# Optimization experiments

Measured on AMD Instinct MI355X. Metric: run time of the kernel, lower is better.

## Reference

```python
import jax, jax.numpy as jnp
import numpy as np

ALPHA = 3.0      # tanhalpha
K = 10           # subgraph_size (overridden to 10 in __init__)
PROP_ALPHA = 0.05
DEPTH = 2        # gcn_depth
NUM_FEAT = 2


def _build_graph(emb1, emb2, w1, b1, w2, b2):
    # MTGNN graph_constructor: directed adjacency + row-wise top-k sparsification
    n1 = jnp.tanh(ALPHA * (emb1 @ w1 + b1))
    n2 = jnp.tanh(ALPHA * (emb2 @ w2 + b2))
    a = n1 @ n2.T - n2 @ n1.T
    adj = jax.nn.relu(jnp.tanh(ALPHA * a))          # [N, N]
    _, idx = jax.lax.top_k(adj, K)                  # keep top-K per row
    N = adj.shape[0]
    mask = jnp.zeros_like(adj).at[jnp.arange(N)[:, None], idx].set(1.0)
    return adj * mask


def _norm_adj(adj):
    a = adj + jnp.eye(adj.shape[0], dtype=adj.dtype)
    return a / a.sum(axis=1, keepdims=True)


def _mixprop(x, a_norm, w, b):
    # x: [B, C, N, L]; multi-hop diffusion then 1x1 conv over stacked hops
    h = x
    outs = [x]
    for _ in range(DEPTH):
        h = PROP_ALPHA * x + (1.0 - PROP_ALPHA) * jnp.einsum('bcwl,vw->bcvl', h, a_norm)
        outs.append(h)
    ho = jnp.concatenate(outs, axis=1)              # [B, (D+1)C, N, L]
    return jnp.einsum('bcnl,oc->bonl', ho, w) + b[None, :, None, None]


def _conv1x1(x, w, b):
    # 1x1 Conv2d over channel dim of [B, C, N, L]
    return jnp.einsum('bcnl,oc->bonl', x, w) + b[None, :, None, None]


def _forward(history_data, node_emb_u, T_i_D_emb, D_i_W_emb,
             gc_emb1, gc_emb2, gc_w1, gc_b1, gc_w2, gc_b2,
             W_emb, b_emb, Wg1, bg1, Wg2, bg2, Wsc, bsc,
             mix1_w, mix1_b, mix2_w, mix2_b,
             Wtf1, btf1, Wtf2, btf2, Wec1, bec1, Wec2, bec2,
             Wfc1, bfc1, Wfc2, bfc2, Wec3, bec3):
    # --- prepare inputs ---
    tid_idx = (history_data[..., NUM_FEAT] * 288.0).astype(jnp.int32)   # [B,T,N]
    diw_idx = history_data[..., NUM_FEAT + 1].astype(jnp.int32)
    tid = T_i_D_emb[tid_idx]                                            # [B,T,N,TE]
    diw = D_i_W_emb[diw_idx]                                            # [B,T,N,TE]
    hd = history_data[..., :NUM_FEAT]                                   # [B,T,N,F]

    adj = _build_graph(gc_emb1, gc_emb2, gc_w1, gc_b1, gc_w2, gc_b2)    # [N,N]

    hd = hd @ W_emb + b_emb                                             # [B,T,N,H]
    B, T, N, H = hd.shape

    # --- decouple gate 1 ---
    nu = jnp.broadcast_to(node_emb_u[None, None], (B, T, N, node_emb_u.shape[-1]))
    g_in = jnp.concatenate([nu, tid, diw], axis=-1)                     # [B,T,N,64]
    gate = jax.nn.sigmoid(jax.nn.relu(g_in @ Wg1 + bg1) @ Wg2 + bg2)    # [B,T,N,H]
    x1 = gate * hd
    x2 = hd - x1
    gated = jnp.concatenate([x1, x2], axis=-1)                          # [B,T,N,2H]

    # start conv acts on the T(=12) dim as channels
    x1 = jax.nn.relu(jnp.einsum('btnh,ot->bonh', x1, Wsc) + bsc[None, :, None, None])
    x2 = jax.nn.relu(jnp.einsum('btnh,ot->bonh', x2, Wsc) + bsc[None, :, None, None])

    aN = _norm_adj(adj)
    aTN = _norm_adj(adj.T)
    outs = []
    for i in range(2):
        H1 = _mixprop(x1, aN, mix1_w[i], mix1_b[i]) + _mixprop(x1, aTN, mix2_w[i], mix2_b[i])
        H2 = _mixprop(x2, aN, mix1_w[i], mix1_b[i]) + _mixprop(x2, aTN, mix2_w[i], mix2_b[i])
        outs.append(H1)
        outs.append(H2)
    out = jnp.concatenate(outs, axis=-1)                                # [B,32,N,4H]

    # TFModule: 2-layer MLP on last dim (dropout = identity in eval)
    x = jax.nn.relu(out @ Wtf1 + btf1) @ Wtf2 + btf2                    # [B,32,N,4H]

    x = jax.nn.relu(_conv1x1(x, Wec1, bec1))                            # [B,128,N,4H]
    x = _conv1x1(x, Wec2, bec2)                                         # [B,12,N,4H]

    fh = jnp.concatenate([gated, x, tid, diw, hd], axis=-1)             # [B,12,N,472]
    f = jax.nn.relu(jax.nn.relu(fh) @ Wfc1 + bfc1) @ Wfc2 + bfc2        # [B,12,N,gap]
    f = _conv1x1(f, Wec3, bec3)                                         # [B,4,N,gap]
    f = jnp.transpose(f, (0, 2, 1, 3)).reshape(B, N, -1)                # [B,N,12]
    return f


def setup_inputs() -> dict:
    key = jax.random.key(0)
    ks = iter(jax.random.split(key, 48))
    def p(*shape, s=0.1):
        return (jax.random.normal(next(ks), shape, jnp.float32) * s)
    B, T, N, F_, H, ND, TE = 8, 12, 1024, 2, 64, 40, 12
    feat = jax.random.normal(next(ks), (B, T, N, F_), jnp.float32)
    tid = jax.random.uniform(next(ks), (B, T, N, 1), jnp.float32)
    diw = jax.random.randint(next(ks), (B, T, N, 1), 0, 7).astype(jnp.float32)
    history_data = jnp.concatenate([feat, tid, diw], axis=-1)
    return {
        'history_data': history_data,
        'node_emb_u': p(N, ND), 'T_i_D_emb': p(288, TE), 'D_i_W_emb': p(7, TE),
        'gc_emb1': p(N, ND), 'gc_emb2': p(N, ND),
        'gc_w1': p(ND, ND), 'gc_b1': jnp.zeros((ND,), jnp.float32),
        'gc_w2': p(ND, ND), 'gc_b2': jnp.zeros((ND,), jnp.float32),
        'W_emb': p(F_, H), 'b_emb': jnp.zeros((H,), jnp.float32),
        'Wg1': p(ND + 2 * TE, 64), 'bg1': jnp.zeros((64,), jnp.float32),
        'Wg2': p(64, H), 'bg2': jnp.zeros((H,), jnp.float32),
        'Wsc': p(32, T), 'bsc': jnp.zeros((32,), jnp.float32),
        'mix1_w': p(2, 32, 96), 'mix1_b': jnp.zeros((2, 32), jnp.float32),
        'mix2_w': p(2, 32, 96), 'mix2_b': jnp.zeros((2, 32), jnp.float32),
        'Wtf1': p(4 * H, 256, s=0.05), 'btf1': jnp.zeros((256,), jnp.float32),
        'Wtf2': p(256, 4 * H, s=0.05), 'btf2': jnp.zeros((4 * H,), jnp.float32),
        'Wec1': p(128, 32), 'bec1': jnp.zeros((128,), jnp.float32),
        'Wec2': p(12, 128), 'bec2': jnp.zeros((12,), jnp.float32),
        'Wfc1': p(472, 512, s=0.05), 'bfc1': jnp.zeros((512,), jnp.float32),
        'Wfc2': p(512, 3, s=0.05), 'bfc2': jnp.zeros((3,), jnp.float32),
        'Wec3': p(4, 12), 'bec3': jnp.zeros((4,), jnp.float32),
    }


def reference(history_data, node_emb_u, T_i_D_emb, D_i_W_emb,
              gc_emb1, gc_emb2, gc_w1, gc_b1, gc_w2, gc_b2,
              W_emb, b_emb, Wg1, bg1, Wg2, bg2, Wsc, bsc,
              mix1_w, mix1_b, mix2_w, mix2_b,
              Wtf1, btf1, Wtf2, btf2, Wec1, bec1, Wec2, bec2,
              Wfc1, bfc1, Wfc2, bfc2, Wec3, bec3):
    return _forward(history_data, node_emb_u, T_i_D_emb, D_i_W_emb,
                    gc_emb1, gc_emb2, gc_w1, gc_b1, gc_w2, gc_b2,
                    W_emb, b_emb, Wg1, bg1, Wg2, bg2, Wsc, bsc,
                    mix1_w, mix1_b, mix2_w, mix2_b,
                    Wtf1, btf1, Wtf2, btf2, Wec1, bec1, Wec2, bec2,
                    Wfc1, bfc1, Wfc2, bfc2, Wec3, bec3)
```

## Files before the change

kernel.cpp:

```cpp
#include <hip/hip_runtime.h>
#include <math.h>

constexpr int ROWS_PER_B = 12 * 1024;

constexpr size_t F_N1 = 0;
constexpr size_t F_N2 = 40960;
constexpr size_t F_ANVAL = 81920;
constexpr size_t F_ROWVAL = 93184;
constexpr size_t F_COLSUM = 103424;
constexpr size_t F_INVCS = 104448;
constexpr size_t F_ATVAL = 105472;
constexpr size_t I_ANIDX = 115712;
constexpr size_t I_ROWIDX = 126976;
constexpr size_t I_COLCNT = 137216;
constexpr size_t I_COLOFF = 138240;
constexpr size_t I_COLFILL = 139265;
constexpr size_t I_ATIDX = 140289;
constexpr size_t F_W1P = 151552;
constexpr size_t F_W2P = 184320;
constexpr size_t F_WFCP = 217088;
constexpr size_t F_WEC1P = 339968;
constexpr size_t F_WEC2P = 342016;
constexpr size_t F_WMWP = 343040;
constexpr size_t GRAPH_FLOATS = 524288;

constexpr size_t PB_GATED = (size_t)ROWS_PER_B * 128 / 2;
constexpr size_t PB_HD = (size_t)ROWS_PER_B * 64 / 2;
constexpr size_t PB_X = (size_t)32 * 1024 * 64 / 2;
constexpr size_t PB_MIX = (size_t)32 * 1024 * 256 / 2;
constexpr size_t PB_TOTAL = PB_GATED + PB_HD + 5 * PB_X + PB_MIX;

typedef __attribute__((ext_vector_type(8))) short bf16x8;
typedef __attribute__((ext_vector_type(4))) float f32x4;

__device__ __forceinline__ unsigned short f2bf(float f) {
    unsigned u = __float_as_uint(f);
    unsigned r = (u + 0x7fffu + ((u >> 16) & 1u)) >> 16;
    return (unsigned short)r;
}
__device__ __forceinline__ float bf2f(unsigned short h) {
    return __uint_as_float((unsigned)h << 16);
}
__device__ __forceinline__ void unpack8(uint4 raw, float* f) {
    f[0] = bf2f((unsigned short)(raw.x & 0xffff)); f[1] = bf2f((unsigned short)(raw.x >> 16));
    f[2] = bf2f((unsigned short)(raw.y & 0xffff)); f[3] = bf2f((unsigned short)(raw.y >> 16));
    f[4] = bf2f((unsigned short)(raw.z & 0xffff)); f[5] = bf2f((unsigned short)(raw.z >> 16));
    f[6] = bf2f((unsigned short)(raw.w & 0xffff)); f[7] = bf2f((unsigned short)(raw.w >> 16));
}
__device__ __forceinline__ uint4 pack8(const float* f) {
    uint4 r;
    r.x = f2bf(f[0]) | ((unsigned)f2bf(f[1]) << 16);
    r.y = f2bf(f[2]) | ((unsigned)f2bf(f[3]) << 16);
    r.z = f2bf(f[4]) | ((unsigned)f2bf(f[5]) << 16);
    r.w = f2bf(f[6]) | ((unsigned)f2bf(f[7]) << 16);
    return r;
}
__device__ __forceinline__ bf16x8 relu8(bf16x8 v) {
#pragma unroll
    for (int j = 0; j < 8; j++) {
        unsigned short u = (unsigned short)v[j];
        v[j] = (short)((u >> 15) ? 0 : u);
    }
    return v;
}


__global__ void k_init(int* cnt, int* fill, float* csum) {
    int t = blockIdx.x * 256 + threadIdx.x;
    if (t < 1024) { cnt[t] = 0; fill[t] = 0; csum[t] = 0.f; }
}

__global__ void k_embed(const float* e1, const float* e2, const float* w1, const float* b1,
                        const float* w2, const float* b2, float* n1, float* n2) {
    int idx = blockIdx.x * 256 + threadIdx.x;
    if (idx >= 81920) return;
    int m = idx / 40960, rem = idx - m * 40960;
    int i = rem / 40, j = rem - i * 40;
    const float* e = m ? e2 : e1;
    const float* w = m ? w2 : w1;
    const float* bv = m ? b2 : b1;
    float a = bv[j];
    for (int k = 0; k < 40; k++) a += e[i * 40 + k] * w[k * 40 + j];
    (m ? n2 : n1)[i * 40 + j] = tanhf(3.0f * a);
}

__global__ __launch_bounds__(256) void k_adj(const float* n1, const float* n2,
        float* aN_val, int* aN_idx, float* row_val, int* row_idx,
        int* col_cnt, float* col_sum) {
    __shared__ float arow[1024];
    __shared__ float n1v[40], n2v[40];
    __shared__ float rv[256];
    __shared__ int ri[256];
    __shared__ float topv[10];
    __shared__ int topi[10];
    int v = blockIdx.x, t = threadIdx.x;
    if (t < 40) { n1v[t] = n1[v * 40 + t]; n2v[t] = n2[v * 40 + t]; }
    __syncthreads();
    for (int j = t; j < 1024; j += 256) {
        float d1 = 0.f, d2 = 0.f;
        for (int k = 0; k < 40; k++) {
            d1 += n1v[k] * n2[j * 40 + k];
            d2 += n2v[k] * n1[j * 40 + k];
        }
        float a = tanhf(3.0f * (d1 - d2));
        arow[j] = a > 0.f ? a : 0.f;
    }
    __syncthreads();
    for (int r = 0; r < 10; r++) {
        float bv = -1.f; int bi = 1 << 30;
        for (int j = t; j < 1024; j += 256) {
            float x = arow[j];
            if (x > bv || (x == bv && j < bi)) { bv = x; bi = j; }
        }
        rv[t] = bv; ri[t] = bi;
        __syncthreads();
        for (int s = 128; s > 0; s >>= 1) {
            if (t < s) {
                float ov = rv[t + s]; int oi = ri[t + s];
                if (ov > rv[t] || (ov == rv[t] && oi < ri[t])) { rv[t] = ov; ri[t] = oi; }
            }
            __syncthreads();
        }
        if (t == 0) { topv[r] = rv[0]; topi[r] = ri[0]; arow[ri[0]] = -1.f; }
        __syncthreads();
    }
    if (t == 0) {
        float s = 1.f;
        for (int r = 0; r < 10; r++) s += topv[r];
        float inv = 1.f / s;
        for (int r = 0; r < 10; r++) {
            aN_idx[v * 11 + r] = topi[r];
            aN_val[v * 11 + r] = topv[r] * inv;
            row_idx[v * 10 + r] = topi[r];
            row_val[v * 10 + r] = topv[r];
            atomicAdd(&col_cnt[topi[r]], 1);
            atomicAdd(&col_sum[topi[r]], topv[r]);
        }
        aN_idx[v * 11 + 10] = v;
        aN_val[v * 11 + 10] = inv;
    }
}

__global__ __launch_bounds__(1024) void k_scan(const int* cnt, int* off,
                                               const float* csum, float* inv) {
    __shared__ int tmp[1024];
    int t = threadIdx.x;
    tmp[t] = cnt[t];
    __syncthreads();
    for (int s = 1; s < 1024; s <<= 1) {
        int v = 0;
        if (t >= s) v = tmp[t - s];
        __syncthreads();
        tmp[t] += v;
        __syncthreads();
    }
    off[t + 1] = tmp[t];
    if (t == 0) off[0] = 0;
    inv[t] = 1.0f / (csum[t] + 1.0f);
}

__global__ void k_scatter(const int* row_idx, const float* row_val, const int* off,
                          int* fill, int* aT_idx, float* aT_val) {
    int e = blockIdx.x * 256 + threadIdx.x;
    if (e >= 10240) return;
    int v = e / 10;
    int j = row_idx[e];
    int pos = off[j] + atomicAdd(&fill[j], 1);
    aT_idx[pos] = v;
    aT_val[pos] = row_val[e];
}

__global__ void k_packw(const float* W, unsigned short* out) {
    int id = blockIdx.x * 256 + threadIdx.x;
    if (id >= 8192) return;
    int lane = id & 63, rest = id >> 6;
    int nb = rest & 15, kb = rest >> 4;
    int krow = kb * 32 + (lane >> 4) * 8;
    int col = nb * 16 + (lane & 15);
    unsigned short v[8];
#pragma unroll
    for (int j = 0; j < 8; j++) v[j] = f2bf(W[(size_t)(krow + j) * 256 + col]);
#pragma unroll
    for (int j = 0; j < 8; j++) out[(size_t)id * 8 + j] = v[j];
}

__global__ void k_packfc(const float* W, unsigned short* out) {
    int id = blockIdx.x * 256 + threadIdx.x;
    if (id >= 30720) return;
    int lane = id & 63, rest = id >> 6;
    int nb = rest & 31, kb = rest >> 5;
    int k0 = kb * 32 + (lane >> 4) * 8;
    int col = nb * 16 + (lane & 15);
    unsigned short v[8];
#pragma unroll
    for (int j = 0; j < 8; j++) {
        int k = k0 + j;
        v[j] = (k < 472) ? f2bf(W[(size_t)k * 512 + col]) : (unsigned short)0;
    }
#pragma unroll
    for (int j = 0; j < 8; j++) out[(size_t)id * 8 + j] = v[j];
}

__global__ void k_packec(const float* W1, const float* W2,
                         unsigned short* o1, unsigned short* o2) {
    int id = blockIdx.x * 256 + threadIdx.x;
    if (id < 512) {
        int mt = id >> 6, lane = id & 63;
        int o = mt * 16 + (lane & 15);
        int c0 = (lane >> 4) * 8;
#pragma unroll
        for (int j = 0; j < 8; j++)
            o1[(size_t)id * 8 + j] = f2bf(W1[o * 32 + c0 + j]);
    } else if (id < 768) {
        int id2 = id - 512;
        int kb = id2 >> 6, lane = id2 & 63;
        int p = lane & 15;
        int k0 = kb * 32 + (lane >> 4) * 8;
#pragma unroll
        for (int j = 0; j < 8; j++)
            o2[(size_t)id2 * 8 + j] = (p < 12) ? f2bf(W2[p * 128 + k0 + j])
                                               : (unsigned short)0;
    }
}

__global__ void k_packmw(const float* mw1, const float* mw2, unsigned short* out) {
    int id = blockIdx.x * 256 + threadIdx.x;
    if (id >= 1536) return;
    int f = id >> 6, lane = id & 63;
    int kb = f >> 2, rt = f & 3;
    int row = rt * 16 + (lane & 15);
    int ph = (kb >= 3) ? 1 : 0;
    int kloc = (kb - ph * 3) * 32 + (lane >> 4) * 8;
    const float* mw = ph ? mw2 : mw1;
#pragma unroll
    for (int j = 0; j < 8; j++)
        out[(size_t)id * 8 + j] = f2bf(mw[row * 96 + kloc + j]);
}


__global__ __launch_bounds__(256) void k_gate(const float* hist, const float* nodeu,
        const float* tide, const float* diwe,
        const float* Wg1, const float* bg1, const float* Wg2, const float* bg2,
        const float* Wemb, const float* bemb, unsigned short* gated, unsigned short* hd_emb) {
    __shared__ float w1[4096], w2[4096];
    __shared__ float gin[4][64], hid[4][64];
    __shared__ float sb1[64], sb2[64], we[128], be[64];
    int t = threadIdx.x;
    for (int i = t; i < 4096; i += 256) { w1[i] = Wg1[i]; w2[i] = Wg2[i]; }
    if (t < 64) { sb1[t] = bg1[t]; sb2[t] = bg2[t]; be[t] = bemb[t]; }
    if (t < 128) we[t] = Wemb[t];
    int r = t >> 6, lane = t & 63;
    int row = blockIdx.x * 4 + r;
    int n = row & 1023;
    const float* hrow = hist + (size_t)row * 4;
    float f0 = hrow[0], f1 = hrow[1];
    int tid_i = (int)(hrow[2] * 288.0f);
    int diw_i = (int)hrow[3];
    float g;
    if (lane < 40) g = nodeu[n * 40 + lane];
    else if (lane < 52) g = tide[tid_i * 12 + lane - 40];
    else g = diwe[diw_i * 12 + lane - 52];
    gin[r][lane] = g;
    __syncthreads();
    float acc = sb1[lane];
    for (int k = 0; k < 64; k++) acc += gin[r][k] * w1[k * 64 + lane];
    hid[r][lane] = acc > 0.f ? acc : 0.f;
    __syncthreads();
    acc = sb2[lane];
    for (int k = 0; k < 64; k++) acc += hid[r][k] * w2[k * 64 + lane];
    float gate = 1.f / (1.f + expf(-acc));
    float hd = f0 * we[lane] + f1 * we[64 + lane] + be[lane];
    float x1 = gate * hd;
    gated[(size_t)row * 128 + lane] = f2bf(x1);
    gated[(size_t)row * 128 + 64 + lane] = f2bf(hd - x1);
    hd_emb[(size_t)row * 64 + lane] = f2bf(hd);
}

__global__ __launch_bounds__(256) void k_wsc(const unsigned short* gated, const float* Wsc,
                                             const float* bsc, unsigned short* xs, int xoff) {
    __shared__ float w[384];
    __shared__ float sb[32];
    int t = threadIdx.x;
    if (t < 384) w[t] = Wsc[t];
    if (t < 32) sb[t] = bsc[t];
    __syncthreads();
    int idx = blockIdx.x * 256 + t;
    int h = idx & 63, n = (idx >> 6) & 1023, b = idx >> 16;
    float xv[12];
#pragma unroll
    for (int tt = 0; tt < 12; tt++)
        xv[tt] = bf2f(gated[(size_t)((b * 12 + tt) * 1024 + n) * 128 + xoff + h]);
#pragma unroll
    for (int o = 0; o < 32; o++) {
        float a = sb[o];
#pragma unroll
        for (int tt = 0; tt < 12; tt++) a += xv[tt] * w[o * 12 + tt];
        xs[(size_t)((b * 32 + o) * 1024 + n) * 64 + h] = f2bf(a > 0.f ? a : 0.f);
    }
}

__global__ __launch_bounds__(256) void k_spmm2(unsigned short* out1, unsigned short* out2,
        const unsigned short* x, const unsigned short* hin1, const unsigned short* hin2,
        const int* aN_idx, const float* aN_val,
        const int* aT_idx, const float* aT_val,
        const int* off, const float* inv_cs) {
    int nper = gridDim.x >> 3;
    int bid = (blockIdx.x & 7) * nper + (blockIdx.x >> 3);
    int t = threadIdx.x;
    int l8 = t & 7, r = t >> 3;
    int g = bid * 32 + r;
    int v = g & 1023, bc = g >> 10;
    size_t rowoff = (size_t)bc * 65536;
    float hv[8];
    const unsigned short* base1 = hin1 + rowoff;
    float s1[8];
#pragma unroll
    for (int j = 0; j < 8; j++) s1[j] = 0.f;
#pragma unroll
    for (int e = 0; e < 11; e++) {
        int w = aN_idx[v * 11 + e];
        float a = aN_val[v * 11 + e];
        uint4 raw = *(const uint4*)(base1 + (size_t)w * 64 + l8 * 8);
        unpack8(raw, hv);
#pragma unroll
        for (int j = 0; j < 8; j++) s1[j] += a * hv[j];
    }
    const unsigned short* base2 = hin2 + rowoff;
    float s2[8];
    {
        uint4 raw = *(const uint4*)(base2 + (size_t)v * 64 + l8 * 8);
        unpack8(raw, s2);
        int e0 = off[v], e1 = off[v + 1];
        for (int e = e0; e < e1; e++) {
            int w = aT_idx[e];
            float a = aT_val[e];
            uint4 rw = *(const uint4*)(base2 + (size_t)w * 64 + l8 * 8);
            unpack8(rw, hv);
#pragma unroll
            for (int j = 0; j < 8; j++) s2[j] += a * hv[j];
        }
        float ic = inv_cs[v];
#pragma unroll
        for (int j = 0; j < 8; j++) s2[j] *= ic;
    }
    uint4 xr = *(const uint4*)(x + (size_t)g * 64 + l8 * 8);
    float xv[8];
    unpack8(xr, xv);
    float o1[8], o2[8];
#pragma unroll
    for (int j = 0; j < 8; j++) {
        float xb = 0.05f * xv[j];
        o1[j] = xb + 0.95f * s1[j];
        o2[j] = xb + 0.95f * s2[j];
    }
    *(uint4*)(out1 + (size_t)g * 64 + l8 * 8) = pack8(o1);
    *(uint4*)(out2 + (size_t)g * 64 + l8 * 8) = pack8(o2);
}

__global__ __launch_bounds__(256) void k_proj(const unsigned short* xs,
        const unsigned short* h1, const unsigned short* h2,
        const unsigned short* h1b, const unsigned short* h2b,
        const unsigned short* mwp, const float* m1b, const float* m2b,
        unsigned short* mix, int xp) {
    __shared__ unsigned short Bf[24 * 64 * 8];
    int t = threadIdx.x;
    int wave = t >> 6, l = t & 63;
    int lr = l & 15, lg = l >> 4;
    int b = blockIdx.x >> 10, n = blockIdx.x & 1023;
#pragma unroll
    for (int i = 0; i < 6; i++) {
        int f = wave * 6 + i;
        int kb = f >> 2, nt = f & 3;
        int ph = (kb >= 3) ? 1 : 0;
        int q = kb - ph * 3;
        const unsigned short* Hq = (q == 0) ? xs : (q == 1 ? (ph ? h1b : h1)
                                                           : (ph ? h2b : h2));
        const unsigned short* src = Hq + ((size_t)(b * 32 + lg * 8) * 1024 + n) * 64
                                       + nt * 16 + lr;
        bf16x8 v;
#pragma unroll
        for (int j = 0; j < 8; j++)
            v[j] = (short)src[(size_t)j * 65536];
        *(bf16x8*)(Bf + ((size_t)f * 64 + l) * 8) = v;
    }
    __syncthreads();
    f32x4 acc[4];
#pragma unroll
    for (int nt = 0; nt < 4; nt++) {
        f32x4 c;
#pragma unroll
        for (int r = 0; r < 4; r++) {
            int row = wave * 16 + lg * 4 + r;
            c[r] = m1b[row] + m2b[row];
        }
        acc[nt] = c;
    }
#pragma unroll
    for (int kb = 0; kb < 6; kb++) {
        bf16x8 af = *(const bf16x8*)(mwp + (size_t)((kb * 4 + wave) * 64 + l) * 8);
#pragma unroll
        for (int nt = 0; nt < 4; nt++) {
            bf16x8 bfv = *(const bf16x8*)(Bf + ((size_t)(kb * 4 + nt) * 64 + l) * 8);
            acc[nt] = __builtin_amdgcn_mfma_f32_16x16x32_bf16(af, bfv, acc[nt], 0, 0, 0);
        }
    }
#pragma unroll
    for (int nt = 0; nt < 4; nt++)
#pragma unroll
        for (int r = 0; r < 4; r++) {
            int row = wave * 16 + lg * 4 + r;
            int i2 = row >> 5, o = row & 31;
            mix[(size_t)((b * 32 + o) * 1024 + n) * 256 + (i2 * 2 + xp) * 64 + nt * 16 + lr]
                = f2bf(acc[nt][r]);
        }
}

__global__ __launch_bounds__(256) void k_tf(unsigned short* mix, const unsigned short* W1p,
                                            const float* B1, const unsigned short* W2p,
                                            const float* B2) {
    __shared__ unsigned short Abuf[32 * 256];
    __shared__ unsigned short Hbuf[32 * 256];
    int t = threadIdx.x;
    int wave = t >> 6, l = t & 63;
    size_t row0 = (size_t)blockIdx.x * 32;
    const uint4* src = (const uint4*)(mix + row0 * 256);
#pragma unroll
    for (int it = 0; it < 4; it++) {
        int f = t + it * 256;
        uint4 raw = src[f];
        int e = f * 8, row = e >> 8, col = e & 255;
        int byte = (row * 512 + col * 2) ^ ((row & 7) << 4);
        *(uint4*)((char*)Abuf + byte) = raw;
    }
    __syncthreads();
    int colg0 = wave * 64;
    int lr = l & 15, lg = l >> 4;
    f32x4 acc[2][4];
#pragma unroll
    for (int nb = 0; nb < 4; nb++) {
        float bv = B1[colg0 + nb * 16 + lr];
        f32x4 c; c[0] = bv; c[1] = bv; c[2] = bv; c[3] = bv;
        acc[0][nb] = c; acc[1][nb] = c;
    }
#pragma unroll
    for (int kb = 0; kb < 8; kb++) {
        int k2 = (kb * 32 + lg * 8) * 2;
        int by0 = (lr * 512 + k2) ^ ((lr & 7) << 4);
        int by1 = ((16 + lr) * 512 + k2) ^ ((lr & 7) << 4);
        bf16x8 a0 = *(const bf16x8*)((char*)Abuf + by0);
        bf16x8 a1 = *(const bf16x8*)((char*)Abuf + by1);
#pragma unroll
        for (int nb = 0; nb < 4; nb++) {
            int nbg = wave * 4 + nb;
            bf16x8 bw = *(const bf16x8*)(W1p + (size_t)((kb * 16 + nbg) * 64 + l) * 8);
            acc[0][nb] = __builtin_amdgcn_mfma_f32_16x16x32_bf16(a0, bw, acc[0][nb], 0, 0, 0);
            acc[1][nb] = __builtin_amdgcn_mfma_f32_16x16x32_bf16(a1, bw, acc[1][nb], 0, 0, 0);
        }
    }
#pragma unroll
    for (int rb = 0; rb < 2; rb++)
#pragma unroll
        for (int nb = 0; nb < 4; nb++)
#pragma unroll
            for (int r = 0; r < 4; r++) {
                int row = rb * 16 + lg * 4 + r;
                int col = colg0 + nb * 16 + lr;
                unsigned short h = f2bf(fmaxf(acc[rb][nb][r], 0.f));
                int byte = (row * 512 + col * 2) ^ ((row & 7) << 4);
                *(unsigned short*)((char*)Hbuf + byte) = h;
            }
    __syncthreads();
#pragma unroll
    for (int nb = 0; nb < 4; nb++) {
        float bv = B2[colg0 + nb * 16 + lr];
        f32x4 c; c[0] = bv; c[1] = bv; c[2] = bv; c[3] = bv;
        acc[0][nb] = c; acc[1][nb] = c;
    }
#pragma unroll
    for (int kb = 0; kb < 8; kb++) {
        int k2 = (kb * 32 + lg * 8) * 2;
        int by0 = (lr * 512 + k2) ^ ((lr & 7) << 4);
        int by1 = ((16 + lr) * 512 + k2) ^ ((lr & 7) << 4);
        bf16x8 a0 = *(const bf16x8*)((char*)Hbuf + by0);
        bf16x8 a1 = *(const bf16x8*)((char*)Hbuf + by1);
#pragma unroll
        for (int nb = 0; nb < 4; nb++) {
            int nbg = wave * 4 + nb;
            bf16x8 bw = *(const bf16x8*)(W2p + (size_t)((kb * 16 + nbg) * 64 + l) * 8);
            acc[0][nb] = __builtin_amdgcn_mfma_f32_16x16x32_bf16(a0, bw, acc[0][nb], 0, 0, 0);
            acc[1][nb] = __builtin_amdgcn_mfma_f32_16x16x32_bf16(a1, bw, acc[1][nb], 0, 0, 0);
        }
    }
#pragma unroll
    for (int rb = 0; rb < 2; rb++)
#pragma unroll
        for (int nb = 0; nb < 4; nb++)
#pragma unroll
            for (int r = 0; r < 4; r++) {
                int row = rb * 16 + lg * 4 + r;
                int col = colg0 + nb * 16 + lr;
                mix[(row0 + row) * 256 + col] = f2bf(acc[rb][nb][r]);
            }
}

__global__ __launch_bounds__(256) void k_ec(const unsigned short* tfo,
        const unsigned short* W1p, const float* B1,
        const unsigned short* W2p, const float* B2, unsigned short* eco) {
    __shared__ unsigned short Hl[4 * 64 * 48];
    int t = threadIdx.x;
    int wave = t >> 6, l = t & 63;
    int lr = l & 15, lg = l >> 4;
    int b = blockIdx.x >> 10, n = blockIdx.x & 1023;
    int lbase = wave * 64;
    unsigned short* myH = Hl + wave * 3072;
    const unsigned short* xb = tfo + ((size_t)(b * 32) * 1024 + n) * 256;
    bf16x8 xf[4];
#pragma unroll
    for (int nt = 0; nt < 4; nt++) {
        int ll = lbase + nt * 16 + lr;
        bf16x8 v;
#pragma unroll
        for (int j = 0; j < 8; j++)
            v[j] = (short)xb[(size_t)(lg * 8 + j) * 262144 + ll];
        xf[nt] = v;
    }
    f32x4 d2[4];
    {
        f32x4 c;
#pragma unroll
        for (int r = 0; r < 4; r++) {
            int p = lg * 4 + r;
            c[r] = (p < 12) ? B2[p] : 0.f;
        }
#pragma unroll
        for (int nt = 0; nt < 4; nt++) d2[nt] = c;
    }
#pragma unroll
    for (int ch = 0; ch < 4; ch++) {
        f32x4 h[2][4];
#pragma unroll
        for (int mt = 0; mt < 2; mt++) {
            f32x4 c;
#pragma unroll
            for (int r = 0; r < 4; r++) c[r] = B1[ch * 32 + mt * 16 + lg * 4 + r];
#pragma unroll
            for (int nt = 0; nt < 4; nt++) h[mt][nt] = c;
        }
#pragma unroll
        for (int mt = 0; mt < 2; mt++) {
            bf16x8 aw = *(const bf16x8*)(W1p + (size_t)((ch * 2 + mt) * 64 + l) * 8);
#pragma unroll
            for (int nt = 0; nt < 4; nt++)
                h[mt][nt] = __builtin_amdgcn_mfma_f32_16x16x32_bf16(aw, xf[nt], h[mt][nt], 0, 0, 0);
        }
#pragma unroll
        for (int mt = 0; mt < 2; mt++)
#pragma unroll
            for (int nt = 0; nt < 4; nt++) {
                unsigned lo = f2bf(fmaxf(h[mt][nt][0], 0.f)) |
                              ((unsigned)f2bf(fmaxf(h[mt][nt][1], 0.f)) << 16);
                unsigned hi = f2bf(fmaxf(h[mt][nt][2], 0.f)) |
                              ((unsigned)f2bf(fmaxf(h[mt][nt][3], 0.f)) << 16);
                uint2 pk; pk.x = lo; pk.y = hi;
                *(uint2*)(myH + (nt * 16 + lr) * 48 + mt * 16 + lg * 4) = pk;
            }
        bf16x8 aw2 = *(const bf16x8*)(W2p + (size_t)(ch * 64 + l) * 8);
#pragma unroll
        for (int nt = 0; nt < 4; nt++) {
            bf16x8 hf = *(const bf16x8*)(myH + (nt * 16 + lr) * 48 + lg * 8);
            d2[nt] = __builtin_amdgcn_mfma_f32_16x16x32_bf16(aw2, hf, d2[nt], 0, 0, 0);
        }
    }
#pragma unroll
    for (int nt = 0; nt < 4; nt++)
#pragma unroll
        for (int r = 0; r < 4; r++) {
            int p = lg * 4 + r;
            if (p < 12) {
                int ll = lbase + nt * 16 + lr;
                eco[((size_t)(b * 12 + p) * 1024 + n) * 256 + ll] = f2bf(d2[nt][r]);
            }
        }
}

__global__ __launch_bounds__(256, 3) void k_fc(const unsigned short* gated,
        const unsigned short* eco, const unsigned short* hd_emb,
        const float* hist, const float* tide, const float* diwe,
        const unsigned short* W1p, const float* B1, const float* W2,
        float* pbuf) {
    int t = threadIdx.x;
    int wave = t >> 6, l = t & 63;
    int lr = l & 15, lg = l >> 4;
    int row0 = blockIdx.x * 16;
    int grow = row0 + lr;
    int n = grow & 1023, bt = grow >> 10;
    int b = bt / 12, tt = bt - b * 12;
    const unsigned short* gptr = gated + (size_t)grow * 128;
    const unsigned short* eptr = eco + (size_t)((b * 12 + tt) * 1024 + n) * 256;
    const unsigned short* hptr = hd_emb + (size_t)grow * 64;
    int tid_i = (int)(hist[(size_t)grow * 4 + 2] * 288.0f);
    int diw_i = (int)hist[(size_t)grow * 4 + 3];
    bf16x8 af[15];
#pragma unroll
    for (int kb = 0; kb < 15; kb++) {
        int off = kb * 32 + lg * 8;
        if (kb <= 3) {
            af[kb] = relu8(*(const bf16x8*)(gptr + off));
        } else if (kb <= 11) {
            af[kb] = relu8(*(const bf16x8*)(eptr + off - 128));
        } else if (kb == 12) {
            bf16x8 v;
#pragma unroll
            for (int j = 0; j < 8; j++) {
                int k = off + j;
                float x;
                if (k < 396) x = tide[tid_i * 12 + k - 384];
                else if (k < 408) x = diwe[diw_i * 12 + k - 396];
                else x = bf2f(hptr[k - 408]);
                v[j] = (short)f2bf(fmaxf(x, 0.f));
            }
            af[kb] = v;
        } else if (kb == 13) {
            af[kb] = relu8(*(const bf16x8*)(hptr + off - 408));
        } else {
            if (lg < 3) af[kb] = relu8(*(const bf16x8*)(hptr + off - 408));
            else {
                bf16x8 z;
#pragma unroll
                for (int j = 0; j < 8; j++) z[j] = 0;
                af[kb] = z;
            }
        }
    }
    __builtin_amdgcn_sched_barrier(0);
    int colg0 = wave * 128;
    f32x4 acc[8];
#pragma unroll
    for (int nb = 0; nb < 8; nb++) {
        float bv = B1[colg0 + nb * 16 + lr];
        f32x4 c; c[0] = bv; c[1] = bv; c[2] = bv; c[3] = bv;
        acc[nb] = c;
    }
#pragma unroll
    for (int kb = 0; kb < 15; kb++) {
#pragma unroll
        for (int nb = 0; nb < 8; nb++) {
            bf16x8 bw = *(const bf16x8*)(W1p + (size_t)((kb * 32 + wave * 8 + nb) * 64 + l) * 8);
            acc[nb] = __builtin_amdgcn_mfma_f32_16x16x32_bf16(af[kb], bw, acc[nb], 0, 0, 0);
        }
    }
    float p[4][3];
#pragma unroll
    for (int r = 0; r < 4; r++) { p[r][0] = 0.f; p[r][1] = 0.f; p[r][2] = 0.f; }
#pragma unroll
    for (int nb = 0; nb < 8; nb++) {
        int col = colg0 + nb * 16 + lr;
        float w0 = W2[col * 3], w1 = W2[col * 3 + 1], w2 = W2[col * 3 + 2];
#pragma unroll
        for (int r = 0; r < 4; r++) {
            float h = fmaxf(acc[nb][r], 0.f);
            p[r][0] += h * w0; p[r][1] += h * w1; p[r][2] += h * w2;
        }
    }
#pragma unroll
    for (int off = 8; off >= 1; off >>= 1)
#pragma unroll
        for (int r = 0; r < 4; r++) {
            p[r][0] += __shfl_xor(p[r][0], off);
            p[r][1] += __shfl_xor(p[r][1], off);
            p[r][2] += __shfl_xor(p[r][2], off);
        }
    if (lr == 0) {
#pragma unroll
        for (int r = 0; r < 4; r++) {
            size_t gr = (size_t)(row0 + lg * 4 + r);
#pragma unroll
            for (int pp = 0; pp < 3; pp++)
                pbuf[gr * 12 + wave * 3 + pp] = p[r][pp];
        }
    }
}

__global__ void k_ec3(const float* pbuf, const float* B2, const float* W, const float* bv,
                      float* out) {
    int idx = blockIdx.x * 256 + threadIdx.x;
    int l = idx % 3;
    int rest = idx / 3;
    int o = rest & 3;
    int n = (rest >> 2) & 1023;
    int b = rest >> 12;
    float s = bv[o];
#pragma unroll
    for (int c = 0; c < 12; c++) {
        const float* pb = pbuf + ((size_t)(b * 12 + c) * 1024 + n) * 12;
        float fv = B2[l] + pb[l] + pb[3 + l] + pb[6 + l] + pb[9 + l];
        s += fv * W[o * 12 + c];
    }
    out[idx] = s;
}

extern "C" void kernel_launch(void* const* d_in, const int* in_sizes, int n_in,
                              void* d_out, int out_size, void* d_ws, size_t ws_size,
                              hipStream_t stream) {
    const float* hist = (const float*)d_in[0];
    const float* node_emb_u = (const float*)d_in[1];
    const float* T_i_D_emb = (const float*)d_in[2];
    const float* D_i_W_emb = (const float*)d_in[3];
    const float* gc_emb1 = (const float*)d_in[4];
    const float* gc_emb2 = (const float*)d_in[5];
    const float* gc_w1 = (const float*)d_in[6];
    const float* gc_b1 = (const float*)d_in[7];
    const float* gc_w2 = (const float*)d_in[8];
    const float* gc_b2 = (const float*)d_in[9];
    const float* W_emb = (const float*)d_in[10];
    const float* b_emb = (const float*)d_in[11];
    const float* Wg1 = (const float*)d_in[12];
    const float* bg1 = (const float*)d_in[13];
    const float* Wg2 = (const float*)d_in[14];
    const float* bg2 = (const float*)d_in[15];
    const float* Wsc = (const float*)d_in[16];
    const float* bsc = (const float*)d_in[17];
    const float* mix1_w = (const float*)d_in[18];
    const float* mix1_b = (const float*)d_in[19];
    const float* mix2_w = (const float*)d_in[20];
    const float* mix2_b = (const float*)d_in[21];
    const float* Wtf1 = (const float*)d_in[22];
    const float* btf1 = (const float*)d_in[23];
    const float* Wtf2 = (const float*)d_in[24];
    const float* btf2 = (const float*)d_in[25];
    const float* Wec1 = (const float*)d_in[26];
    const float* bec1 = (const float*)d_in[27];
    const float* Wec2 = (const float*)d_in[28];
    const float* bec2 = (const float*)d_in[29];
    const float* Wfc1 = (const float*)d_in[30];
    const float* bfc1 = (const float*)d_in[31];
    const float* Wfc2 = (const float*)d_in[32];
    const float* bfc2 = (const float*)d_in[33];
    const float* Wec3 = (const float*)d_in[34];
    const float* bec3 = (const float*)d_in[35];

    float* ws = (float*)d_ws;
    float* n1 = ws + F_N1;
    float* n2 = ws + F_N2;
    float* aN_val = ws + F_ANVAL;
    float* row_val = ws + F_ROWVAL;
    float* col_sum = ws + F_COLSUM;
    float* inv_cs = ws + F_INVCS;
    float* aT_val = ws + F_ATVAL;
    int* aN_idx = (int*)(ws + I_ANIDX);
    int* row_idx = (int*)(ws + I_ROWIDX);
    int* col_cnt = (int*)(ws + I_COLCNT);
    int* col_off = (int*)(ws + I_COLOFF);
    int* col_fill = (int*)(ws + I_COLFILL);
    int* aT_idx = (int*)(ws + I_ATIDX);
    unsigned short* w1p = (unsigned short*)(ws + F_W1P);
    unsigned short* w2p = (unsigned short*)(ws + F_W2P);
    unsigned short* wfcp = (unsigned short*)(ws + F_WFCP);
    unsigned short* wec1p = (unsigned short*)(ws + F_WEC1P);
    unsigned short* wec2p = (unsigned short*)(ws + F_WEC2P);
    unsigned short* wmwp = (unsigned short*)(ws + F_WMWP);

    size_t avail = ws_size / 4;
    int CB = 8;
    while (CB > 1 && GRAPH_FLOATS + (size_t)CB * PB_TOTAL > avail) CB >>= 1;
    int nchunk = 8 / CB;

    unsigned short* gated = (unsigned short*)(ws + GRAPH_FLOATS);
    unsigned short* hd_emb = (unsigned short*)(ws + GRAPH_FLOATS + (size_t)CB * PB_GATED);
    unsigned short* xs = (unsigned short*)(ws + GRAPH_FLOATS + (size_t)CB * (PB_GATED + PB_HD));
    unsigned short* h1 = xs + (size_t)CB * PB_X * 2;
    unsigned short* h2 = h1 + (size_t)CB * PB_X * 2;
    unsigned short* h1b = h2 + (size_t)CB * PB_X * 2;
    unsigned short* h2b = h1b + (size_t)CB * PB_X * 2;
    unsigned short* mix = h2b + (size_t)CB * PB_X * 2;
    unsigned short* eco = xs;
    float* fbuf = (float*)h2b;

    k_init<<<4, 256, 0, stream>>>(col_cnt, col_fill, col_sum);
    k_embed<<<320, 256, 0, stream>>>(gc_emb1, gc_emb2, gc_w1, gc_b1, gc_w2, gc_b2, n1, n2);
    k_adj<<<1024, 256, 0, stream>>>(n1, n2, aN_val, aN_idx, row_val, row_idx, col_cnt, col_sum);
    k_scan<<<1, 1024, 0, stream>>>(col_cnt, col_off, col_sum, inv_cs);
    k_scatter<<<40, 256, 0, stream>>>(row_idx, row_val, col_off, col_fill, aT_idx, aT_val);
    k_packw<<<32, 256, 0, stream>>>(Wtf1, w1p);
    k_packw<<<32, 256, 0, stream>>>(Wtf2, w2p);
    k_packfc<<<120, 256, 0, stream>>>(Wfc1, wfcp);
    k_packec<<<3, 256, 0, stream>>>(Wec1, Wec2, wec1p, wec2p);
    k_packmw<<<6, 256, 0, stream>>>(mix1_w, mix2_w, wmwp);

    for (int ch = 0; ch < nchunk; ch++) {
        const float* hist_c = hist + (size_t)ch * CB * ROWS_PER_B * 4;
        float* out_c = (float*)d_out + (size_t)ch * CB * ROWS_PER_B;

        k_gate<<<CB * 3072, 256, 0, stream>>>(hist_c, node_emb_u, T_i_D_emb, D_i_W_emb,
                                              Wg1, bg1, Wg2, bg2, W_emb, b_emb, gated, hd_emb);
        for (int xp = 0; xp < 2; xp++) {
            k_wsc<<<CB * 256, 256, 0, stream>>>(gated, Wsc, bsc, xs, xp * 64);
            k_spmm2<<<CB * 1024, 256, 0, stream>>>(h1, h1b, xs, xs, xs,
                                                   aN_idx, aN_val, aT_idx, aT_val,
                                                   col_off, inv_cs);
            k_spmm2<<<CB * 1024, 256, 0, stream>>>(h2, h2b, xs, h1, h1b,
                                                   aN_idx, aN_val, aT_idx, aT_val,
                                                   col_off, inv_cs);
            k_proj<<<CB * 1024, 256, 0, stream>>>(xs, h1, h2, h1b, h2b,
                                                  wmwp, mix1_b, mix2_b, mix, xp);
        }
        k_tf<<<CB * 1024, 256, 0, stream>>>(mix, w1p, btf1, w2p, btf2);
        k_ec<<<CB * 1024, 256, 0, stream>>>(mix, wec1p, bec1, wec2p, bec2, eco);
        k_fc<<<CB * 768, 256, 0, stream>>>(gated, eco, hd_emb, hist_c, T_i_D_emb, D_i_W_emb,
                                           wfcp, bfc1, Wfc2, fbuf);
        k_ec3<<<CB * 48, 256, 0, stream>>>(fbuf, bfc2, Wec3, bec3, out_c);
    }
}
```

Measured before the change: 1.186 ms.

## Split FC input gathering into separate staging kernel with MFMA-packed layout

```diff
diff --git a/kernel.cpp b/kernel.cpp
--- a/kernel.cpp
+++ b/kernel.cpp
@@ -28,7 +28,8 @@
 constexpr size_t PB_HD = (size_t)ROWS_PER_B * 64 / 2;
 constexpr size_t PB_X = (size_t)32 * 1024 * 64 / 2;
 constexpr size_t PB_MIX = (size_t)32 * 1024 * 256 / 2;
-constexpr size_t PB_TOTAL = PB_GATED + PB_HD + 5 * PB_X + PB_MIX;
+constexpr size_t PB_APK = (size_t)768 * 15 * 64 * 8 / 2;
+constexpr size_t PB_TOTAL = PB_GATED + PB_HD + 5 * PB_X + PB_MIX + PB_APK;
 
 typedef __attribute__((ext_vector_type(8))) short bf16x8;
 typedef __attribute__((ext_vector_type(4))) float f32x4;
@@ -583,56 +584,56 @@
         }
 }
 
-__global__ __launch_bounds__(256, 3) void k_fc(const unsigned short* gated,
+__global__ __launch_bounds__(256) void k_stage(const unsigned short* gated,
         const unsigned short* eco, const unsigned short* hd_emb,
         const float* hist, const float* tide, const float* diwe,
+        unsigned short* apk) {
+    int id = blockIdx.x * 256 + threadIdx.x;
+    int lane = id & 63, rest = id >> 6;
+    int rg = rest / 15, kb = rest - rg * 15;
+    int lr = lane & 15, lg = lane >> 4;
+    int grow = rg * 16 + lr;
+    int n = grow & 1023, bt = grow >> 10;
+    int b = bt / 12, tt = bt - b * 12;
+    int off = kb * 32 + lg * 8;
+    bf16x8 v;
+    if (kb <= 3) {
+        v = relu8(*(const bf16x8*)(gated + (size_t)grow * 128 + off));
+    } else if (kb <= 11) {
+        v = relu8(*(const bf16x8*)(eco + (size_t)((b * 12 + tt) * 1024 + n) * 256 + off - 128));
+    } else if (kb == 12) {
+        int tid_i = (int)(hist[(size_t)grow * 4 + 2] * 288.0f);
+        int diw_i = (int)hist[(size_t)grow * 4 + 3];
+        const unsigned short* hptr = hd_emb + (size_t)grow * 64;
+#pragma unroll
+        for (int j = 0; j < 8; j++) {
+            int k = off + j;
+            float x;
+            if (k < 396) x = tide[tid_i * 12 + k - 384];
+            else if (k < 408) x = diwe[diw_i * 12 + k - 396];
+            else x = bf2f(hptr[k - 408]);
+            v[j] = (short)f2bf(fmaxf(x, 0.f));
+        }
+    } else if (kb == 13) {
+        v = relu8(*(const bf16x8*)(hd_emb + (size_t)grow * 64 + off - 408));
+    } else {
+        if (lg < 3) v = relu8(*(const bf16x8*)(hd_emb + (size_t)grow * 64 + off - 408));
+        else {
+#pragma unroll
+            for (int j = 0; j < 8; j++) v[j] = 0;
+        }
+    }
+    *(bf16x8*)(apk + (size_t)id * 8) = v;
+}
+
+__global__ __launch_bounds__(256) void k_fc(const unsigned short* apk,
         const unsigned short* W1p, const float* B1, const float* W2,
         float* pbuf) {
     int t = threadIdx.x;
     int wave = t >> 6, l = t & 63;
     int lr = l & 15, lg = l >> 4;
-    int row0 = blockIdx.x * 16;
-    int grow = row0 + lr;
-    int n = grow & 1023, bt = grow >> 10;
-    int b = bt / 12, tt = bt - b * 12;
-    const unsigned short* gptr = gated + (size_t)grow * 128;
-    const unsigned short* eptr = eco + (size_t)((b * 12 + tt) * 1024 + n) * 256;
-    const unsigned short* hptr = hd_emb + (size_t)grow * 64;
-    int tid_i = (int)(hist[(size_t)grow * 4 + 2] * 288.0f);
-    int diw_i = (int)hist[(size_t)grow * 4 + 3];
-    bf16x8 af[15];
-#pragma unroll
-    for (int kb = 0; kb < 15; kb++) {
-        int off = kb * 32 + lg * 8;
-        if (kb <= 3) {
-            af[kb] = relu8(*(const bf16x8*)(gptr + off));
-        } else if (kb <= 11) {
-            af[kb] = relu8(*(const bf16x8*)(eptr + off - 128));
-        } else if (kb == 12) {
-            bf16x8 v;
-#pragma unroll
-            for (int j = 0; j < 8; j++) {
-                int k = off + j;
-                float x;
-                if (k < 396) x = tide[tid_i * 12 + k - 384];
-                else if (k < 408) x = diwe[diw_i * 12 + k - 396];
-                else x = bf2f(hptr[k - 408]);
-                v[j] = (short)f2bf(fmaxf(x, 0.f));
-            }
-            af[kb] = v;
-        } else if (kb == 13) {
-            af[kb] = relu8(*(const bf16x8*)(hptr + off - 408));
-        } else {
-            if (lg < 3) af[kb] = relu8(*(const bf16x8*)(hptr + off - 408));
-            else {
-                bf16x8 z;
-#pragma unroll
-                for (int j = 0; j < 8; j++) z[j] = 0;
-                af[kb] = z;
-            }
-        }
-    }
-    __builtin_amdgcn_sched_barrier(0);
+    int rg = blockIdx.x;
+    int row0 = rg * 16;
     int colg0 = wave * 128;
     f32x4 acc[8];
 #pragma unroll
@@ -643,10 +644,11 @@
     }
 #pragma unroll
     for (int kb = 0; kb < 15; kb++) {
+        bf16x8 af = *(const bf16x8*)(apk + (size_t)((rg * 15 + kb) * 64 + l) * 8);
 #pragma unroll
         for (int nb = 0; nb < 8; nb++) {
             bf16x8 bw = *(const bf16x8*)(W1p + (size_t)((kb * 32 + wave * 8 + nb) * 64 + l) * 8);
-            acc[nb] = __builtin_amdgcn_mfma_f32_16x16x32_bf16(af[kb], bw, acc[nb], 0, 0, 0);
+            acc[nb] = __builtin_amdgcn_mfma_f32_16x16x32_bf16(af, bw, acc[nb], 0, 0, 0);
         }
     }
     float p[4][3];
@@ -773,6 +775,7 @@
     unsigned short* h1b = h2 + (size_t)CB * PB_X * 2;
     unsigned short* h2b = h1b + (size_t)CB * PB_X * 2;
     unsigned short* mix = h2b + (size_t)CB * PB_X * 2;
+    unsigned short* apk = mix + (size_t)CB * PB_MIX * 2;
     unsigned short* eco = xs;
     float* fbuf = (float*)h2b;
 
@@ -806,8 +809,9 @@
         }
         k_tf<<<CB * 1024, 256, 0, stream>>>(mix, w1p, btf1, w2p, btf2);
         k_ec<<<CB * 1024, 256, 0, stream>>>(mix, wec1p, bec1, wec2p, bec2, eco);
-        k_fc<<<CB * 768, 256, 0, stream>>>(gated, eco, hd_emb, hist_c, T_i_D_emb, D_i_W_emb,
-                                           wfcp, bfc1, Wfc2, fbuf);
+        k_stage<<<CB * 2880, 256, 0, stream>>>(gated, eco, hd_emb, hist_c,
+                                               T_i_D_emb, D_i_W_emb, apk);
+        k_fc<<<CB * 768, 256, 0, stream>>>(apk, wfcp, bfc1, Wfc2, fbuf);
         k_ec3<<<CB * 48, 256, 0, stream>>>(fbuf, bfc2, Wec3, bec3, out_c);
     }
 }
```

After: 1.185 ms. About the same (-0.1%).
